# Optimization experiments

Measured on AMD Instinct MI355X. Metric: run time of the kernel, lower is better.

The kernel has to match this reference:

```python
import jax, jax.numpy as jnp
import numpy as np

N, E, F, H, A, C, NC, L, AH = 50000, 800000, 768, 256, 128, 128, 7, 2, 4

def _ln(x, g, b):
    m = jnp.mean(x, axis=-1, keepdims=True)
    v = jnp.var(x, axis=-1, keepdims=True)
    return (x - m) / jnp.sqrt(v + 1e-5) * g + b

def setup_inputs() -> dict:
    key = jax.random.key(0)
    ks = jax.random.split(key, 32)
    s = 0.02
    d = {}
    d['x'] = jax.random.normal(ks[0], (N, F), jnp.float32)
    d['edge_index'] = jax.random.randint(ks[1], (2, E), 0, N, jnp.int32)
    d['W_in'] = jax.random.normal(ks[2], (F, H), jnp.float32) * s
    d['b_in'] = jnp.zeros((H,), jnp.float32)
    d['gin_W1'] = jax.random.normal(ks[3], (L, H, H), jnp.float32) * s
    d['gin_b1'] = jnp.zeros((L, H), jnp.float32)
    d['gin_lng'] = jnp.ones((L, H), jnp.float32)
    d['gin_lnb'] = jnp.zeros((L, H), jnp.float32)
    d['gin_W2'] = jax.random.normal(ks[4], (L, H, H), jnp.float32) * s
    d['gin_b2'] = jnp.zeros((L, H), jnp.float32)
    d['eps'] = jnp.zeros((L,), jnp.float32)
    d['ln_g'] = jnp.ones((L, H), jnp.float32)
    d['ln_b'] = jnp.zeros((L, H), jnp.float32)
    d['att_W1'] = jax.random.normal(ks[5], (AH, H, A), jnp.float32) * s
    d['att_b1'] = jnp.zeros((AH, A), jnp.float32)
    d['att_W2'] = jax.random.normal(ks[6], (AH, A), jnp.float32) * s
    d['att_b2'] = jnp.zeros((AH,), jnp.float32)
    d['Wc1'] = jax.random.normal(ks[7], (H, C), jnp.float32) * s
    d['bc1'] = jnp.zeros((C,), jnp.float32)
    d['lnc1_g'] = jnp.ones((C,), jnp.float32)
    d['lnc1_b'] = jnp.zeros((C,), jnp.float32)
    d['Wc2'] = jax.random.normal(ks[8], (C, C // 2), jnp.float32) * s
    d['bc2'] = jnp.zeros((C // 2,), jnp.float32)
    d['lnc2_g'] = jnp.ones((C // 2,), jnp.float32)
    d['lnc2_b'] = jnp.zeros((C // 2,), jnp.float32)
    d['Wc3'] = jax.random.normal(ks[9], (C // 2, NC), jnp.float32) * s
    d['bc3'] = jnp.zeros((NC,), jnp.float32)
    return d

def reference(x, edge_index, W_in, b_in, gin_W1, gin_b1, gin_lng, gin_lnb, gin_W2, gin_b2, eps, ln_g, ln_b, att_W1, att_b1, att_W2, att_b2, Wc1, bc1, lnc1_g, lnc1_b, Wc2, bc2, lnc2_g, lnc2_b, Wc3, bc3):
    src, dst = edge_index[0], edge_index[1]
    # input projection (use_residual and input_dim != gnn_hidden)
    h = x @ W_in + b_in  # [N,H]
    for i in range(L):
        agg = jax.ops.segment_sum(h[src], dst, num_segments=N)  # GIN sum aggregation
        m = (1.0 + eps[i]) * h + agg
        m = _ln(m @ gin_W1[i] + gin_b1[i], gin_lng[i], gin_lnb[i])
        m = jax.nn.relu(m) @ gin_W2[i] + gin_b2[i]
        hn = jax.nn.relu(_ln(m, ln_g[i], ln_b[i]))
        h = hn + h  # residual (shapes match)
    # multi-head attention pooling, softmax over node dim
    s = jnp.tanh(jnp.einsum('nd,kda->kna', h, att_W1) + att_b1[:, None, :])  # [AH,N,A]
    logits = jnp.einsum('kna,ka->kn', s, att_W2) + att_b2[:, None]  # [AH,N]
    a = jax.nn.softmax(logits, axis=1)  # [AH,N]
    z = jnp.einsum('kn,nd->kd', a, h)  # [AH,H]
    z_agg = jnp.mean(z, axis=0)  # [H]
    attn = a.T  # [N,AH]
    # classifier (full variant)
    c = jax.nn.relu(_ln(z_agg @ Wc1 + bc1, lnc1_g, lnc1_b))
    c = jax.nn.relu(_ln(c @ Wc2 + bc2, lnc2_g, lnc2_b))
    probs = jax.nn.softmax(c @ Wc3 + bc3, axis=0)
    return probs, attn
```

## Files before the change

### kernel.cpp

```cpp
#include <hip/hip_runtime.h>
#include <math.h>

#define NN 50000
#define NE 800000
#define FF 768
#define HH 256

typedef __attribute__((ext_vector_type(8))) short short8;
typedef __attribute__((ext_vector_type(4))) float f32x4;

__device__ inline unsigned short f2bf(float f) {
  unsigned u = __float_as_uint(f);
  u = u + 0x7fffu + ((u >> 16) & 1u);
  return (unsigned short)(u >> 16);
}
__device__ inline float bf2f(unsigned short b) {
  return __uint_as_float(((unsigned)b) << 16);
}

__global__ void k_count(const int* __restrict__ dstv, int* __restrict__ deg) {
  int e = blockIdx.x * 256 + threadIdx.x;
  if (e < NE) atomicAdd(&deg[dstv[e]], 1);
}

__global__ void k_scan(const int* __restrict__ deg, int* __restrict__ rowptr) {
  const int CH = 49;
  int tid = threadIdx.x;
  int lane = tid & 63, w = tid >> 6;
  int base = tid * CH;
  int sum = 0;
  for (int i = 0; i < CH; i++) {
    int idx = base + i;
    if (idx < NN) sum += deg[idx];
  }
  int incl = sum;
  for (int off = 1; off < 64; off <<= 1) {
    int tv = __shfl_up(incl, off, 64);
    if (lane >= off) incl += tv;
  }
  __shared__ int ws[16];
  if (lane == 63) ws[w] = incl;
  __syncthreads();
  if (tid == 0) {
    int c = 0;
    for (int i = 0; i < 16; i++) { int tv = ws[i]; ws[i] = c; c += tv; }
  }
  __syncthreads();
  int run = ws[w] + (incl - sum);
  if (tid == 0) rowptr[0] = 0;
  for (int i = 0; i < CH; i++) {
    int idx = base + i;
    if (idx < NN) { run += deg[idx]; rowptr[idx + 1] = run; }
  }
}

__global__ void k_scatter(const int* __restrict__ srcv, const int* __restrict__ dstv,
                          int* __restrict__ cursor, int* __restrict__ csr_src) {
  int e = blockIdx.x * 256 + threadIdx.x;
  if (e < NE) {
    int d = dstv[e];
    int pos = atomicAdd(&cursor[d], 1);
    csr_src[pos] = srcv[e];
  }
}

__global__ void k_agg(const unsigned short* __restrict__ hb, const int* __restrict__ rowptr,
                      const int* __restrict__ csr_src, const float* __restrict__ eps,
                      int layer, unsigned short* __restrict__ mb) {
  int node = (blockIdx.x * blockDim.x + threadIdx.x) >> 6;
  int lane = threadIdx.x & 63;
  if (node >= NN) return;
  int beg = rowptr[node], end = rowptr[node + 1];
  const ushort4* hv = (const ushort4*)hb;
  float ax = 0.f, ay = 0.f, az = 0.f, aw = 0.f;
  for (int e = beg; e < end; ++e) {
    int s = csr_src[e];
    ushort4 v = hv[(size_t)s * 64 + lane];
    ax += bf2f(v.x); ay += bf2f(v.y); az += bf2f(v.z); aw += bf2f(v.w);
  }
  float ep = 1.0f + eps[layer];
  ushort4 h0 = hv[(size_t)node * 64 + lane];
  ax += ep * bf2f(h0.x); ay += ep * bf2f(h0.y);
  az += ep * bf2f(h0.z); aw += ep * bf2f(h0.w);
  ushort4 o;
  o.x = f2bf(ax); o.y = f2bf(ay); o.z = f2bf(az); o.w = f2bf(aw);
  *(ushort4*)&mb[(size_t)node * 256 + lane * 4] = o;
}

__global__ void k_tcast(const float* __restrict__ src0, unsigned short* __restrict__ dst0,
                        int R, int C) {
  const float* src = src0 + (size_t)blockIdx.z * R * C;
  unsigned short* dst = dst0 + (size_t)blockIdx.z * R * C;
  __shared__ float tile[32][33];
  int bx = blockIdx.x * 32, by = blockIdx.y * 32;
  int tx = threadIdx.x & 31, ty = threadIdx.x >> 5;
  for (int i = 0; i < 32; i += 8) {
    int r = by + ty + i, c = bx + tx;
    tile[ty + i][tx] = (r < R && c < C) ? src[(size_t)r * C + c] : 0.f;
  }
  __syncthreads();
  for (int i = 0; i < 32; i += 8) {
    int c = bx + ty + i, r = by + tx;
    if (c < C && r < R) dst[(size_t)c * R + r] = f2bf(tile[tx][ty + i]);
  }
}

__global__ __launch_bounds__(256) void k_mmff(
    const float* __restrict__ x, const unsigned short* __restrict__ Bt,
    const float* __restrict__ bias, float* __restrict__ outf,
    unsigned short* __restrict__ outb) {
  __shared__ unsigned short As[64 * 264];
  int t = threadIdx.x, lane = t & 63, wave = t >> 6;
  int row0 = blockIdx.x * 64;
  int m16 = lane & 15, kq = lane >> 4;
  f32x4 acc[4][4];
#pragma unroll
  for (int i = 0; i < 4; i++)
#pragma unroll
    for (int j = 0; j < 4; j++) acc[i][j] = (f32x4)(0.f);
  int sr = t >> 5;
  int sc = (t & 31) * 8;

  for (int kc = 0; kc < FF; kc += 256) {
    if (kc) __syncthreads();
#pragma unroll
    for (int j = 0; j < 8; j++) {
      int rr = j * 8 + sr;
      int gr = row0 + rr; if (gr >= NN) gr = NN - 1;
      const float* xp = x + (size_t)gr * FF + kc + sc;
      float4 f0 = *(const float4*)xp;
      float4 f1 = *(const float4*)(xp + 4);
      short8 v;
      v[0] = (short)f2bf(f0.x); v[1] = (short)f2bf(f0.y);
      v[2] = (short)f2bf(f0.z); v[3] = (short)f2bf(f0.w);
      v[4] = (short)f2bf(f1.x); v[5] = (short)f2bf(f1.y);
      v[6] = (short)f2bf(f1.z); v[7] = (short)f2bf(f1.w);
      *(short8*)&As[rr * 264 + sc] = v;
    }
    __syncthreads();
#pragma unroll
    for (int k0 = 0; k0 < 256; k0 += 32) {
      short8 a[4], b[4];
#pragma unroll
      for (int rt = 0; rt < 4; rt++)
        a[rt] = *(const short8*)&As[(rt * 16 + m16) * 264 + k0 + kq * 8];
#pragma unroll
      for (int ct = 0; ct < 4; ct++)
        b[ct] = *(const short8*)&Bt[(size_t)(wave * 64 + ct * 16 + m16) * FF + kc + k0 + kq * 8];
#pragma unroll
      for (int rt = 0; rt < 4; rt++)
#pragma unroll
        for (int ct = 0; ct < 4; ct++)
          acc[rt][ct] = __builtin_amdgcn_mfma_f32_16x16x32_bf16(a[rt], b[ct], acc[rt][ct], 0, 0, 0);
    }
  }
  int colbase = wave * 64 + m16;
  float bv[4];
#pragma unroll
  for (int ct = 0; ct < 4; ct++) bv[ct] = bias[colbase + ct * 16];
#pragma unroll
  for (int rt = 0; rt < 4; rt++)
#pragma unroll
    for (int reg = 0; reg < 4; reg++) {
      int r = row0 + rt * 16 + kq * 4 + reg;
      if (r < NN) {
#pragma unroll
        for (int ct = 0; ct < 4; ct++) {
          float v = acc[rt][ct][reg] + bv[ct];
          outf[(size_t)r * 256 + colbase + ct * 16] = v;
          outb[(size_t)r * 256 + colbase + ct * 16] = f2bf(v);
        }
      }
    }
}

template <int EPI, bool WF>
__global__ __launch_bounds__(256) void k_mmh(
    const unsigned short* __restrict__ Ab, const unsigned short* __restrict__ Bt,
    const float* __restrict__ bias, const float* __restrict__ g,
    const float* __restrict__ be, const float* __restrict__ resid,
    float* __restrict__ outf, unsigned short* __restrict__ outb) {
  __shared__ unsigned short As[64 * 264];
  __shared__ float redS[4][64];
  __shared__ float redQ[4][64];
  __shared__ float mvM[64], mvI[64];
  int t = threadIdx.x, lane = t & 63, wave = t >> 6;
  int row0 = blockIdx.x * 64;
  int sr = t >> 5, sc = (t & 31) * 8;
#pragma unroll
  for (int j = 0; j < 8; j++) {
    int rr = j * 8 + sr;
    int gr = row0 + rr; if (gr >= NN) gr = NN - 1;
    *(float4*)&As[rr * 264 + sc] = *(const float4*)&Ab[(size_t)gr * 256 + sc];
  }
  __syncthreads();
  int m16 = lane & 15, kq = lane >> 4;
  f32x4 acc[4][4];
#pragma unroll
  for (int i = 0; i < 4; i++)
#pragma unroll
    for (int j = 0; j < 4; j++) acc[i][j] = (f32x4)(0.f);
#pragma unroll
  for (int k0 = 0; k0 < 256; k0 += 32) {
    short8 a[4], b[4];
#pragma unroll
    for (int rt = 0; rt < 4; rt++)
      a[rt] = *(const short8*)&As[(rt * 16 + m16) * 264 + k0 + kq * 8];
#pragma unroll
    for (int ct = 0; ct < 4; ct++)
      b[ct] = *(const short8*)&Bt[(size_t)(wave * 64 + ct * 16 + m16) * 256 + k0 + kq * 8];
#pragma unroll
    for (int rt = 0; rt < 4; rt++)
#pragma unroll
      for (int ct = 0; ct < 4; ct++)
        acc[rt][ct] = __builtin_amdgcn_mfma_f32_16x16x32_bf16(a[rt], b[ct], acc[rt][ct], 0, 0, 0);
  }

  int colbase = wave * 64 + m16;
  float bv[4];
#pragma unroll
  for (int ct = 0; ct < 4; ct++) bv[ct] = bias[colbase + ct * 16];

  float s[4][4], q[4][4];
#pragma unroll
  for (int rt = 0; rt < 4; rt++)
#pragma unroll
    for (int reg = 0; reg < 4; reg++) { s[rt][reg] = 0.f; q[rt][reg] = 0.f; }
#pragma unroll
  for (int rt = 0; rt < 4; rt++)
#pragma unroll
    for (int ct = 0; ct < 4; ct++)
#pragma unroll
      for (int reg = 0; reg < 4; reg++) {
        float v = acc[rt][ct][reg] + bv[ct];
        acc[rt][ct][reg] = v;
        s[rt][reg] += v;
        q[rt][reg] += v * v;
      }
#pragma unroll
  for (int off = 1; off < 16; off <<= 1) {
#pragma unroll
    for (int rt = 0; rt < 4; rt++)
#pragma unroll
      for (int reg = 0; reg < 4; reg++) {
        s[rt][reg] += __shfl_xor(s[rt][reg], off, 64);
        q[rt][reg] += __shfl_xor(q[rt][reg], off, 64);
      }
  }
  if (m16 == 0) {
#pragma unroll
    for (int rt = 0; rt < 4; rt++)
#pragma unroll
      for (int reg = 0; reg < 4; reg++) {
        redS[wave][rt * 16 + kq * 4 + reg] = s[rt][reg];
        redQ[wave][rt * 16 + kq * 4 + reg] = q[rt][reg];
      }
  }
  __syncthreads();
  if (t < 64) {
    float ss = redS[0][t] + redS[1][t] + redS[2][t] + redS[3][t];
    float qq = redQ[0][t] + redQ[1][t] + redQ[2][t] + redQ[3][t];
    float mean = ss * (1.f / 256.f);
    float var = qq * (1.f / 256.f) - mean * mean;
    mvM[t] = mean;
    mvI[t] = rsqrtf(var + 1e-5f);
  }
  __syncthreads();
  float gv[4], bev[4];
#pragma unroll
  for (int ct = 0; ct < 4; ct++) { gv[ct] = g[colbase + ct * 16]; bev[ct] = be[colbase + ct * 16]; }
#pragma unroll
  for (int rt = 0; rt < 4; rt++)
#pragma unroll
    for (int reg = 0; reg < 4; reg++) {
      int rr = rt * 16 + kq * 4 + reg;
      int r = row0 + rr;
      if (r >= NN) continue;
      float mean = mvM[rr], inv = mvI[rr];
#pragma unroll
      for (int ct = 0; ct < 4; ct++) {
        int col = colbase + ct * 16;
        float val = fmaxf((acc[rt][ct][reg] - mean) * inv * gv[ct] + bev[ct], 0.f);
        if (EPI == 2) {
          val += resid[(size_t)r * 256 + col];
          if (WF) outf[(size_t)r * 256 + col] = val;
        }
        outb[(size_t)r * 256 + col] = f2bf(val);
      }
    }
}

__global__ __launch_bounds__(256) void k_att(const unsigned short* __restrict__ hb,
    const unsigned short* __restrict__ W1T, const float* __restrict__ b1,
    const float* __restrict__ W2, const float* __restrict__ b2,
    float* __restrict__ logitsT) {
  __shared__ unsigned short As[64 * 264];
  int t = threadIdx.x, lane = t & 63, wave = t >> 6;
  int row0 = blockIdx.x * 64;
  int sr = t >> 5, sc = (t & 31) * 8;
#pragma unroll
  for (int j = 0; j < 8; j++) {
    int rr = j * 8 + sr;
    int gr = row0 + rr; if (gr >= NN) gr = NN - 1;
    *(float4*)&As[rr * 264 + sc] = *(const float4*)&hb[(size_t)gr * 256 + sc];
  }
  __syncthreads();
  int m16 = lane & 15, kq = lane >> 4;
  f32x4 acc[4][8];
#pragma unroll
  for (int i = 0; i < 4; i++)
#pragma unroll
    for (int j = 0; j < 8; j++) acc[i][j] = (f32x4)(0.f);
#pragma unroll
  for (int k0 = 0; k0 < 256; k0 += 32) {
    short8 a[4];
#pragma unroll
    for (int rt = 0; rt < 4; rt++)
      a[rt] = *(const short8*)&As[(rt * 16 + m16) * 264 + k0 + kq * 8];
#pragma unroll
    for (int ct = 0; ct < 8; ct++) {
      short8 b = *(const short8*)&W1T[(size_t)(wave * 128 + ct * 16 + m16) * 256 + k0 + kq * 8];
#pragma unroll
      for (int rt = 0; rt < 4; rt++)
        acc[rt][ct] = __builtin_amdgcn_mfma_f32_16x16x32_bf16(a[rt], b, acc[rt][ct], 0, 0, 0);
    }
  }
  const float* b1k = b1 + wave * 128;
  const float* w2k = W2 + wave * 128;
  float p[4][4];
#pragma unroll
  for (int rt = 0; rt < 4; rt++)
#pragma unroll
    for (int reg = 0; reg < 4; reg++) p[rt][reg] = 0.f;
#pragma unroll
  for (int ct = 0; ct < 8; ct++) {
    int col = ct * 16 + m16;
    float b1v = b1k[col], w2v = w2k[col];
#pragma unroll
    for (int rt = 0; rt < 4; rt++)
#pragma unroll
      for (int reg = 0; reg < 4; reg++) {
        float xv = acc[rt][ct][reg] + b1v;
        xv = fminf(fmaxf(xv, -10.f), 10.f);
        float ex = __expf(2.f * xv);
        p[rt][reg] += (ex - 1.f) / (ex + 1.f) * w2v;
      }
  }
#pragma unroll
  for (int off = 1; off < 16; off <<= 1)
#pragma unroll
    for (int rt = 0; rt < 4; rt++)
#pragma unroll
      for (int reg = 0; reg < 4; reg++) p[rt][reg] += __shfl_xor(p[rt][reg], off, 64);
  if (m16 == 0) {
    float b2v = b2[wave];
#pragma unroll
    for (int rt = 0; rt < 4; rt++)
#pragma unroll
      for (int reg = 0; reg < 4; reg++) {
        int r = row0 + rt * 16 + kq * 4 + reg;
        if (r < NN) logitsT[(size_t)wave * NN + r] = p[rt][reg] + b2v;
      }
  }
}

__global__ void k_smax1(const float* __restrict__ logitsT, float* __restrict__ pmax,
                        float* __restrict__ psum) {
  int k = blockIdx.y;
  int tid = threadIdx.x;
  const float* L = logitsT + (size_t)k * NN;
  __shared__ float sm[256];
  float mx = -1e30f;
  for (int i = blockIdx.x * 256 + tid; i < NN; i += 128 * 256) mx = fmaxf(mx, L[i]);
  sm[tid] = mx; __syncthreads();
  for (int o = 128; o >= 1; o >>= 1) { if (tid < o) sm[tid] = fmaxf(sm[tid], sm[tid + o]); __syncthreads(); }
  float bmax = sm[0];
  __syncthreads();
  float s = 0.f;
  for (int i = blockIdx.x * 256 + tid; i < NN; i += 128 * 256) s += __expf(L[i] - bmax);
  sm[tid] = s; __syncthreads();
  for (int o = 128; o >= 1; o >>= 1) { if (tid < o) sm[tid] += sm[tid + o]; __syncthreads(); }
  if (tid == 0) { pmax[k * 128 + blockIdx.x] = bmax; psum[k * 128 + blockIdx.x] = sm[0]; }
}

__global__ void k_smax2(const float* __restrict__ pmax, const float* __restrict__ psum,
                        float* __restrict__ gs) {
  int k = blockIdx.x;
  int tid = threadIdx.x;
  __shared__ float sm[128], sv[128];
  float m = pmax[k * 128 + tid];
  sm[tid] = m; __syncthreads();
  for (int o = 64; o >= 1; o >>= 1) { if (tid < o) sm[tid] = fmaxf(sm[tid], sm[tid + o]); __syncthreads(); }
  float gm = sm[0];
  __syncthreads();
  sv[tid] = psum[k * 128 + tid] * __expf(m - gm);
  __syncthreads();
  for (int o = 64; o >= 1; o >>= 1) { if (tid < o) sv[tid] += sv[tid + o]; __syncthreads(); }
  if (tid == 0) { gs[k * 2] = gm; gs[k * 2 + 1] = sv[0]; }
}

__global__ void k_attnz(const float* __restrict__ logitsT, const float* __restrict__ gs,
                        const unsigned short* __restrict__ hb, float* __restrict__ out_attn,
                        float* __restrict__ z) {
  int n0 = blockIdx.x * 128;
  int tid = threadIdx.x;
  __shared__ float a[4][128];
  for (int i = tid; i < 512; i += 256) {
    int k = i >> 7, n = i & 127;
    float v = 0.f;
    if (n0 + n < NN) v = __expf(logitsT[(size_t)k * NN + n0 + n] - gs[k * 2]) / gs[k * 2 + 1];
    a[k][n] = v;
  }
  __syncthreads();
  for (int i = tid; i < 512; i += 256) {
    int n = i >> 2, k = i & 3;
    if (n0 + n < NN) out_attn[(size_t)(n0 + n) * 4 + k] = a[k][n];
  }
  float z0 = 0.f, z1 = 0.f, z2 = 0.f, z3 = 0.f;
  int d = tid;
  int nmax = NN - n0; if (nmax > 128) nmax = 128;
  for (int n = 0; n < nmax; n++) {
    float hv = bf2f(hb[(size_t)(n0 + n) * 256 + d]);
    z0 += a[0][n] * hv; z1 += a[1][n] * hv; z2 += a[2][n] * hv; z3 += a[3][n] * hv;
  }
  atomicAdd(&z[0 * 256 + d], z0);
  atomicAdd(&z[1 * 256 + d], z1);
  atomicAdd(&z[2 * 256 + d], z2);
  atomicAdd(&z[3 * 256 + d], z3);
}

__global__ void k_cls(const float* __restrict__ z, const float* __restrict__ Wc1,
                      const float* __restrict__ bc1, const float* __restrict__ g1,
                      const float* __restrict__ b1, const float* __restrict__ Wc2,
                      const float* __restrict__ bc2, const float* __restrict__ g2,
                      const float* __restrict__ b2, const float* __restrict__ Wc3,
                      const float* __restrict__ bc3, float* __restrict__ out) {
  int tid = threadIdx.x;
  __shared__ float za[256];
  __shared__ float buf[256];
  __shared__ float c1s[128];
  __shared__ float c2s[64];
  za[tid] = 0.25f * (z[tid] + z[256 + tid] + z[512 + tid] + z[768 + tid]);
  __syncthreads();
  float v1 = 0.f;
  if (tid < 128) {
    for (int d = 0; d < 256; d++) v1 += za[d] * Wc1[d * 128 + tid];
    v1 += bc1[tid];
  }
  buf[tid] = (tid < 128) ? v1 : 0.f; __syncthreads();
  for (int o = 128; o >= 1; o >>= 1) { if (tid < o) buf[tid] += buf[tid + o]; __syncthreads(); }
  float mean1 = buf[0] * (1.f / 128.f);
  __syncthreads();
  buf[tid] = (tid < 128) ? (v1 - mean1) * (v1 - mean1) : 0.f; __syncthreads();
  for (int o = 128; o >= 1; o >>= 1) { if (tid < o) buf[tid] += buf[tid + o]; __syncthreads(); }
  float inv1 = rsqrtf(buf[0] * (1.f / 128.f) + 1e-5f);
  __syncthreads();
  if (tid < 128) c1s[tid] = fmaxf((v1 - mean1) * inv1 * g1[tid] + b1[tid], 0.f);
  __syncthreads();
  float v2 = 0.f;
  if (tid < 64) {
    for (int d = 0; d < 128; d++) v2 += c1s[d] * Wc2[d * 64 + tid];
    v2 += bc2[tid];
  }
  buf[tid] = (tid < 64) ? v2 : 0.f; __syncthreads();
  for (int o = 128; o >= 1; o >>= 1) { if (tid < o) buf[tid] += buf[tid + o]; __syncthreads(); }
  float mean2 = buf[0] * (1.f / 64.f);
  __syncthreads();
  buf[tid] = (tid < 64) ? (v2 - mean2) * (v2 - mean2) : 0.f; __syncthreads();
  for (int o = 128; o >= 1; o >>= 1) { if (tid < o) buf[tid] += buf[tid + o]; __syncthreads(); }
  float inv2 = rsqrtf(buf[0] * (1.f / 64.f) + 1e-5f);
  __syncthreads();
  if (tid < 64) c2s[tid] = fmaxf((v2 - mean2) * inv2 * g2[tid] + b2[tid], 0.f);
  __syncthreads();
  if (tid < 7) {
    float l = 0.f;
    for (int d = 0; d < 64; d++) l += c2s[d] * Wc3[d * 7 + tid];
    buf[tid] = l + bc3[tid];
  }
  __syncthreads();
  if (tid == 0) {
    float mx = -1e30f;
    for (int i = 0; i < 7; i++) mx = fmaxf(mx, buf[i]);
    float s = 0.f;
    for (int i = 0; i < 7; i++) s += __expf(buf[i] - mx);
    for (int i = 0; i < 7; i++) out[i] = __expf(buf[i] - mx) / s;
  }
}

extern "C" void kernel_launch(void* const* d_in, const int* in_sizes, int n_in,
                              void* d_out, int out_size, void* d_ws, size_t ws_size,
                              hipStream_t stream) {
  const float* x       = (const float*)d_in[0];
  const int*   ei      = (const int*)d_in[1];
  const float* W_in    = (const float*)d_in[2];
  const float* b_in    = (const float*)d_in[3];
  const float* gin_W1  = (const float*)d_in[4];
  const float* gin_b1  = (const float*)d_in[5];
  const float* gin_lng = (const float*)d_in[6];
  const float* gin_lnb = (const float*)d_in[7];
  const float* gin_W2  = (const float*)d_in[8];
  const float* gin_b2  = (const float*)d_in[9];
  const float* eps     = (const float*)d_in[10];
  const float* ln_g    = (const float*)d_in[11];
  const float* ln_b    = (const float*)d_in[12];
  const float* att_W1  = (const float*)d_in[13];
  const float* att_b1  = (const float*)d_in[14];
  const float* att_W2  = (const float*)d_in[15];
  const float* att_b2  = (const float*)d_in[16];
  const float* Wc1     = (const float*)d_in[17];
  const float* bc1     = (const float*)d_in[18];
  const float* lnc1_g  = (const float*)d_in[19];
  const float* lnc1_b  = (const float*)d_in[20];
  const float* Wc2     = (const float*)d_in[21];
  const float* bc2     = (const float*)d_in[22];
  const float* lnc2_g  = (const float*)d_in[23];
  const float* lnc2_b  = (const float*)d_in[24];
  const float* Wc3     = (const float*)d_in[25];
  const float* bc3     = (const float*)d_in[26];
  float* out = (float*)d_out;
  (void)in_sizes; (void)n_in; (void)out_size; (void)ws_size;

  char* wsb = (char*)d_ws;
  size_t off = 0;
  auto alloc = [&](size_t bytes) {
    char* p = wsb + off;
    off += (bytes + 255) & ~(size_t)255;
    return p;
  };
  float*          h       = (float*)alloc((size_t)NN * HH * 4);
  unsigned short* hb      = (unsigned short*)alloc((size_t)NN * HH * 2);
  unsigned short* mb1     = (unsigned short*)alloc((size_t)NN * HH * 2);
  unsigned short* mb2     = (unsigned short*)alloc((size_t)NN * HH * 2);
  unsigned short* WinT    = (unsigned short*)alloc((size_t)HH * FF * 2);
  unsigned short* g1T     = (unsigned short*)alloc((size_t)2 * HH * HH * 2);
  unsigned short* g2T     = (unsigned short*)alloc((size_t)2 * HH * HH * 2);
  unsigned short* aW1T    = (unsigned short*)alloc((size_t)4 * 128 * HH * 2);
  float*          logitsT = (float*)alloc((size_t)4 * NN * 4);
  int*            deg     = (int*)alloc((size_t)NN * 4);
  int*            rowptr  = (int*)alloc((size_t)(NN + 1) * 4);
  int*            cursor  = (int*)alloc((size_t)NN * 4);
  int*            csr_src = (int*)alloc((size_t)NE * 4);
  float*          pmax    = (float*)alloc(4 * 128 * 4);
  float*          psum    = (float*)alloc(4 * 128 * 4);
  float*          gs      = (float*)alloc(8 * 4);
  float*          z       = (float*)alloc(4 * 256 * 4);

  const int* srcv = ei;
  const int* dstv = ei + NE;

  k_tcast<<<dim3((HH + 31) / 32, (FF + 31) / 32, 1), 256, 0, stream>>>(W_in, WinT, FF, HH);
  k_tcast<<<dim3(8, 8, 2), 256, 0, stream>>>(gin_W1, g1T, HH, HH);
  k_tcast<<<dim3(8, 8, 2), 256, 0, stream>>>(gin_W2, g2T, HH, HH);
  k_tcast<<<dim3(4, 8, 4), 256, 0, stream>>>(att_W1, aW1T, HH, 128);

  hipMemsetAsync(deg, 0, (size_t)NN * 4, stream);
  hipMemsetAsync(z, 0, 4 * 256 * 4, stream);
  k_count<<<(NE + 255) / 256, 256, 0, stream>>>(dstv, deg);
  k_scan<<<1, 1024, 0, stream>>>(deg, rowptr);
  hipMemcpyAsync(cursor, rowptr, (size_t)NN * 4, hipMemcpyDeviceToDevice, stream);
  k_scatter<<<(NE + 255) / 256, 256, 0, stream>>>(srcv, dstv, cursor, csr_src);

  int gblocks = (NN + 63) / 64;
  k_mmff<<<gblocks, 256, 0, stream>>>(x, WinT, b_in, h, hb);

  for (int l = 0; l < 2; l++) {
    k_agg<<<(NN + 3) / 4, 256, 0, stream>>>(hb, rowptr, csr_src, eps, l, mb1);
    k_mmh<1, true><<<gblocks, 256, 0, stream>>>(mb1, g1T + (size_t)l * HH * HH,
        gin_b1 + l * HH, gin_lng + l * HH, gin_lnb + l * HH, nullptr, nullptr, mb2);
    if (l == 0)
      k_mmh<2, true><<<gblocks, 256, 0, stream>>>(mb2, g2T + (size_t)l * HH * HH,
          gin_b2 + l * HH, ln_g + l * HH, ln_b + l * HH, h, h, hb);
    else
      k_mmh<2, false><<<gblocks, 256, 0, stream>>>(mb2, g2T + (size_t)l * HH * HH,
          gin_b2 + l * HH, ln_g + l * HH, ln_b + l * HH, h, nullptr, hb);
  }

  k_att<<<gblocks, 256, 0, stream>>>(hb, aW1T, att_b1, att_W2, att_b2, logitsT);
  k_smax1<<<dim3(128, 4), 256, 0, stream>>>(logitsT, pmax, psum);
  k_smax2<<<4, 128, 0, stream>>>(pmax, psum, gs);
  k_attnz<<<(NN + 127) / 128, 256, 0, stream>>>(logitsT, gs, hb, out + 7, z);
  k_cls<<<1, 256, 0, stream>>>(z, Wc1, bc1, lnc1_g, lnc1_b, Wc2, bc2, lnc2_g, lnc2_b,
                               Wc3, bc3, out);
}
```

Measured before the change: 1.010 ms.

## Fuse GIN MLP GEMMs and attention scoring into one kernel, stage B in LDS

Each GIN layer's two GEMMs, with their LayerNorm and ReLU epilogues, now run in one kernel that keeps the intermediate activation in LDS instead of writing and rereading mb2. The last layer also computes the attention logits from the same tile, so the separate k_att kernel and its reread of hb go away. Weight tiles are now staged through LDS, with an XOR swizzle in the fused kernel, and the next tile is register-prefetched while the current one is consumed. The input-projection GEMM is restructured the same way with 32-wide K chunks. This cuts global traffic and kernel launches, at the cost of more barriers per block and LDS atomics for the per-head logit reduction.

```diff
diff --git a/kernel.cpp b/kernel.cpp
--- a/kernel.cpp
+++ b/kernel.cpp
@@ -105,11 +105,12 @@
   }
 }
 
-__global__ __launch_bounds__(256) void k_mmff(
+__global__ __launch_bounds__(256) void k_mmff0(
     const float* __restrict__ x, const unsigned short* __restrict__ Bt,
     const float* __restrict__ bias, float* __restrict__ outf,
     unsigned short* __restrict__ outb) {
-  __shared__ unsigned short As[64 * 264];
+  __shared__ unsigned short As[64 * 40];
+  __shared__ unsigned short Bs[256 * 40];
   int t = threadIdx.x, lane = t & 63, wave = t >> 6;
   int row0 = blockIdx.x * 64;
   int m16 = lane & 15, kq = lane >> 4;
@@ -118,249 +119,361 @@
   for (int i = 0; i < 4; i++)
 #pragma unroll
     for (int j = 0; j < 4; j++) acc[i][j] = (f32x4)(0.f);
-  int sr = t >> 5;
-  int sc = (t & 31) * 8;
-
-  for (int kc = 0; kc < FF; kc += 256) {
-    if (kc) __syncthreads();
+  int arow = t >> 2, ac = t & 3;
+  int agr = row0 + arow; if (agr >= NN) agr = NN - 1;
+  float4 pa0, pa1, pb[4];
+  {
+    const float* Af = x + (size_t)agr * FF + ac * 8;
+    pa0 = *(const float4*)Af;
+    pa1 = *(const float4*)(Af + 4);
+#pragma unroll
+    for (int it = 0; it < 4; it++) {
+      int idx = t + it * 256;
+      int br = idx >> 2, bc = idx & 3;
+      pb[it] = *(const float4*)&Bt[(size_t)br * FF + bc * 8];
+    }
+  }
+  for (int kc = 0; kc < 24; kc++) {
+    short8 v;
+    v[0] = (short)f2bf(pa0.x); v[1] = (short)f2bf(pa0.y);
+    v[2] = (short)f2bf(pa0.z); v[3] = (short)f2bf(pa0.w);
+    v[4] = (short)f2bf(pa1.x); v[5] = (short)f2bf(pa1.y);
+    v[6] = (short)f2bf(pa1.z); v[7] = (short)f2bf(pa1.w);
+    *(short8*)&As[arow * 40 + ac * 8] = v;
+#pragma unroll
+    for (int it = 0; it < 4; it++) {
+      int idx = t + it * 256;
+      int br = idx >> 2, bc = idx & 3;
+      *(float4*)&Bs[br * 40 + bc * 8] = pb[it];
+    }
+    if (kc < 23) {
+      int k0 = (kc + 1) * 32;
+      const float* Af = x + (size_t)agr * FF + k0 + ac * 8;
+      pa0 = *(const float4*)Af;
+      pa1 = *(const float4*)(Af + 4);
+#pragma unroll
+      for (int it = 0; it < 4; it++) {
+        int idx = t + it * 256;
+        int br = idx >> 2, bc = idx & 3;
+        pb[it] = *(const float4*)&Bt[(size_t)br * FF + k0 + bc * 8];
+      }
+    }
+    __syncthreads();
+    short8 a[4], b[4];
+#pragma unroll
+    for (int rt = 0; rt < 4; rt++) a[rt] = *(const short8*)&As[(rt * 16 + m16) * 40 + kq * 8];
+#pragma unroll
+    for (int ct = 0; ct < 4; ct++)
+      b[ct] = *(const short8*)&Bs[(wave * 64 + ct * 16 + m16) * 40 + kq * 8];
+#pragma unroll
+    for (int rt = 0; rt < 4; rt++)
+#pragma unroll
+      for (int ct = 0; ct < 4; ct++)
+        acc[rt][ct] = __builtin_amdgcn_mfma_f32_16x16x32_bf16(a[rt], b[ct], acc[rt][ct], 0, 0, 0);
+    __syncthreads();
+  }
+  int colbase = wave * 64 + m16;
+  float bv[4];
+#pragma unroll
+  for (int ct = 0; ct < 4; ct++) bv[ct] = bias[colbase + ct * 16];
+#pragma unroll
+  for (int rt = 0; rt < 4; rt++)
+#pragma unroll
+    for (int reg = 0; reg < 4; reg++) {
+      int r = row0 + rt * 16 + kq * 4 + reg;
+      if (r < NN) {
+#pragma unroll
+        for (int ct = 0; ct < 4; ct++) {
+          float vv = acc[rt][ct][reg] + bv[ct];
+          outf[(size_t)r * 256 + colbase + ct * 16] = vv;
+          outb[(size_t)r * 256 + colbase + ct * 16] = f2bf(vv);
+        }
+      }
+    }
+}
+
+__device__ __forceinline__ void gemm_k256(
+    const unsigned short* __restrict__ Bt, const unsigned short* __restrict__ T1,
+    unsigned short* __restrict__ Bs, f32x4 (&acc)[4][4],
+    int t, int wave, int m16, int kq) {
+  int r4 = t >> 2, slot = t & 3;
+  float4 pf[4];
+#pragma unroll
+  for (int i = 0; i < 4; i++) {
+    int row = i * 64 + r4;
+    pf[i] = *(const float4*)&Bt[(size_t)row * 256 + slot * 8];
+  }
+#pragma unroll
+  for (int kc = 0; kc < 8; kc++) {
+#pragma unroll
+    for (int i = 0; i < 4; i++) {
+      int row = i * 64 + r4;
+      int s2 = slot ^ ((row >> 1) & 3);
+      *(float4*)((char*)Bs + row * 64 + s2 * 16) = pf[i];
+    }
+    if (kc < 7) {
+#pragma unroll
+      for (int i = 0; i < 4; i++) {
+        int row = i * 64 + r4;
+        pf[i] = *(const float4*)&Bt[(size_t)row * 256 + (kc + 1) * 32 + slot * 8];
+      }
+    }
+    __syncthreads();
+    short8 a[4], b[4];
+#pragma unroll
+    for (int rt = 0; rt < 4; rt++)
+      a[rt] = *(const short8*)&T1[(rt * 16 + m16) * 264 + kc * 32 + kq * 8];
+#pragma unroll
+    for (int ct = 0; ct < 4; ct++) {
+      int brow = wave * 64 + ct * 16 + m16;
+      int s2 = kq ^ ((brow >> 1) & 3);
+      b[ct] = *(const short8*)((const char*)Bs + brow * 64 + s2 * 16);
+    }
+#pragma unroll
+    for (int rt = 0; rt < 4; rt++)
+#pragma unroll
+      for (int ct = 0; ct < 4; ct++)
+        acc[rt][ct] = __builtin_amdgcn_mfma_f32_16x16x32_bf16(a[rt], b[ct], acc[rt][ct], 0, 0, 0);
+    __syncthreads();
+  }
+}
+
+template <bool WF, bool ATT>
+__global__ __launch_bounds__(256) void k_fused(
+    const unsigned short* __restrict__ Ab,
+    const unsigned short* __restrict__ B1t, const float* __restrict__ bias1,
+    const float* __restrict__ g1v, const float* __restrict__ be1,
+    const unsigned short* __restrict__ B2t, const float* __restrict__ bias2,
+    const float* __restrict__ g2v, const float* __restrict__ be2,
+    const float* __restrict__ resid, float* __restrict__ outf,
+    unsigned short* __restrict__ outb,
+    const unsigned short* __restrict__ aW1T, const float* __restrict__ ab1,
+    const float* __restrict__ aW2v, const float* __restrict__ ab2,
+    float* __restrict__ logitsT) {
+  __shared__ unsigned short T1[64 * 264];
+  __shared__ unsigned short Bs[256 * 32];
+  __shared__ float redS[4][64];
+  __shared__ float redQ[4][64];
+  __shared__ float mvM[64], mvI[64];
+  __shared__ float lg[4][64];
+  int t = threadIdx.x, lane = t & 63, wave = t >> 6;
+  int row0 = blockIdx.x * 64;
+  int m16 = lane & 15, kq = lane >> 4;
+  int colbase = wave * 64 + m16;
+
+  {
+    int sr = t >> 5, sc = (t & 31) * 8;
 #pragma unroll
     for (int j = 0; j < 8; j++) {
       int rr = j * 8 + sr;
       int gr = row0 + rr; if (gr >= NN) gr = NN - 1;
-      const float* xp = x + (size_t)gr * FF + kc + sc;
-      float4 f0 = *(const float4*)xp;
-      float4 f1 = *(const float4*)(xp + 4);
-      short8 v;
-      v[0] = (short)f2bf(f0.x); v[1] = (short)f2bf(f0.y);
-      v[2] = (short)f2bf(f0.z); v[3] = (short)f2bf(f0.w);
-      v[4] = (short)f2bf(f1.x); v[5] = (short)f2bf(f1.y);
-      v[6] = (short)f2bf(f1.z); v[7] = (short)f2bf(f1.w);
-      *(short8*)&As[rr * 264 + sc] = v;
-    }
-    __syncthreads();
-#pragma unroll
-    for (int k0 = 0; k0 < 256; k0 += 32) {
-      short8 a[4], b[4];
+      *(float4*)&T1[rr * 264 + sc] = *(const float4*)&Ab[(size_t)gr * 256 + sc];
+    }
+  }
+
+  f32x4 acc[4][4];
+#pragma unroll
+  for (int i = 0; i < 4; i++)
+#pragma unroll
+    for (int j = 0; j < 4; j++) acc[i][j] = (f32x4)(0.f);
+  gemm_k256(B1t, T1, Bs, acc, t, wave, m16, kq);
+
+  {
+    float bv[4];
+#pragma unroll
+    for (int ct = 0; ct < 4; ct++) bv[ct] = bias1[colbase + ct * 16];
+    float s[4][4], q[4][4];
+#pragma unroll
+    for (int rt = 0; rt < 4; rt++)
+#pragma unroll
+      for (int reg = 0; reg < 4; reg++) { s[rt][reg] = 0.f; q[rt][reg] = 0.f; }
+#pragma unroll
+    for (int rt = 0; rt < 4; rt++)
+#pragma unroll
+      for (int ct = 0; ct < 4; ct++)
+#pragma unroll
+        for (int reg = 0; reg < 4; reg++) {
+          float v = acc[rt][ct][reg] + bv[ct];
+          acc[rt][ct][reg] = v;
+          s[rt][reg] += v;
+          q[rt][reg] += v * v;
+        }
+#pragma unroll
+    for (int off = 1; off < 16; off <<= 1) {
 #pragma unroll
       for (int rt = 0; rt < 4; rt++)
-        a[rt] = *(const short8*)&As[(rt * 16 + m16) * 264 + k0 + kq * 8];
+#pragma unroll
+        for (int reg = 0; reg < 4; reg++) {
+          s[rt][reg] += __shfl_xor(s[rt][reg], off, 64);
+          q[rt][reg] += __shfl_xor(q[rt][reg], off, 64);
+        }
+    }
+    if (m16 == 0) {
+#pragma unroll
+      for (int rt = 0; rt < 4; rt++)
+#pragma unroll
+        for (int reg = 0; reg < 4; reg++) {
+          redS[wave][rt * 16 + kq * 4 + reg] = s[rt][reg];
+          redQ[wave][rt * 16 + kq * 4 + reg] = q[rt][reg];
+        }
+    }
+    __syncthreads();
+    if (t < 64) {
+      float ss = redS[0][t] + redS[1][t] + redS[2][t] + redS[3][t];
+      float qq = redQ[0][t] + redQ[1][t] + redQ[2][t] + redQ[3][t];
+      float mean = ss * (1.f / 256.f);
+      float var = qq * (1.f / 256.f) - mean * mean;
+      mvM[t] = mean;
+      mvI[t] = rsqrtf(var + 1e-5f);
+    }
+    __syncthreads();
+    float gv[4], bev[4];
+#pragma unroll
+    for (int ct = 0; ct < 4; ct++) { gv[ct] = g1v[colbase + ct * 16]; bev[ct] = be1[colbase + ct * 16]; }
+#pragma unroll
+    for (int rt = 0; rt < 4; rt++)
+#pragma unroll
+      for (int reg = 0; reg < 4; reg++) {
+        int rr = rt * 16 + kq * 4 + reg;
+        float mean = mvM[rr], inv = mvI[rr];
+#pragma unroll
+        for (int ct = 0; ct < 4; ct++) {
+          float val = fmaxf((acc[rt][ct][reg] - mean) * inv * gv[ct] + bev[ct], 0.f);
+          T1[rr * 264 + colbase + ct * 16] = f2bf(val);
+        }
+      }
+    __syncthreads();
+  }
+
+#pragma unroll
+  for (int i = 0; i < 4; i++)
+#pragma unroll
+    for (int j = 0; j < 4; j++) acc[i][j] = (f32x4)(0.f);
+  gemm_k256(B2t, T1, Bs, acc, t, wave, m16, kq);
+
+  {
+    float bv[4];
+#pragma unroll
+    for (int ct = 0; ct < 4; ct++) bv[ct] = bias2[colbase + ct * 16];
+    float s[4][4], q[4][4];
+#pragma unroll
+    for (int rt = 0; rt < 4; rt++)
+#pragma unroll
+      for (int reg = 0; reg < 4; reg++) { s[rt][reg] = 0.f; q[rt][reg] = 0.f; }
+#pragma unroll
+    for (int rt = 0; rt < 4; rt++)
 #pragma unroll
       for (int ct = 0; ct < 4; ct++)
-        b[ct] = *(const short8*)&Bt[(size_t)(wave * 64 + ct * 16 + m16) * FF + kc + k0 + kq * 8];
+#pragma unroll
+        for (int reg = 0; reg < 4; reg++) {
+          float v = acc[rt][ct][reg] + bv[ct];
+          acc[rt][ct][reg] = v;
+          s[rt][reg] += v;
+          q[rt][reg] += v * v;
+        }
+#pragma unroll
+    for (int off = 1; off < 16; off <<= 1) {
 #pragma unroll
       for (int rt = 0; rt < 4; rt++)
 #pragma unroll
-        for (int ct = 0; ct < 4; ct++)
-          acc[rt][ct] = __builtin_amdgcn_mfma_f32_16x16x32_bf16(a[rt], b[ct], acc[rt][ct], 0, 0, 0);
-    }
-  }
-  int colbase = wave * 64 + m16;
-  float bv[4];
-#pragma unroll
-  for (int ct = 0; ct < 4; ct++) bv[ct] = bias[colbase + ct * 16];
-#pragma unroll
-  for (int rt = 0; rt < 4; rt++)
-#pragma unroll
-    for (int reg = 0; reg < 4; reg++) {
-      int r = row0 + rt * 16 + kq * 4 + reg;
-      if (r < NN) {
+        for (int reg = 0; reg < 4; reg++) {
+          s[rt][reg] += __shfl_xor(s[rt][reg], off, 64);
+          q[rt][reg] += __shfl_xor(q[rt][reg], off, 64);
+        }
+    }
+    if (m16 == 0) {
+#pragma unroll
+      for (int rt = 0; rt < 4; rt++)
+#pragma unroll
+        for (int reg = 0; reg < 4; reg++) {
+          redS[wave][rt * 16 + kq * 4 + reg] = s[rt][reg];
+          redQ[wave][rt * 16 + kq * 4 + reg] = q[rt][reg];
+        }
+    }
+    __syncthreads();
+    if (t < 64) {
+      float ss = redS[0][t] + redS[1][t] + redS[2][t] + redS[3][t];
+      float qq = redQ[0][t] + redQ[1][t] + redQ[2][t] + redQ[3][t];
+      float mean = ss * (1.f / 256.f);
+      float var = qq * (1.f / 256.f) - mean * mean;
+      mvM[t] = mean;
+      mvI[t] = rsqrtf(var + 1e-5f);
+    }
+    __syncthreads();
+    float gv[4], bev[4];
+#pragma unroll
+    for (int ct = 0; ct < 4; ct++) { gv[ct] = g2v[colbase + ct * 16]; bev[ct] = be2[colbase + ct * 16]; }
+#pragma unroll
+    for (int rt = 0; rt < 4; rt++)
+#pragma unroll
+      for (int reg = 0; reg < 4; reg++) {
+        int rr = rt * 16 + kq * 4 + reg;
+        int r = row0 + rr;
+        float mean = mvM[rr], inv = mvI[rr];
 #pragma unroll
         for (int ct = 0; ct < 4; ct++) {
-          float v = acc[rt][ct][reg] + bv[ct];
-          outf[(size_t)r * 256 + colbase + ct * 16] = v;
-          outb[(size_t)r * 256 + colbase + ct * 16] = f2bf(v);
+          int col = colbase + ct * 16;
+          float val = fmaxf((acc[rt][ct][reg] - mean) * inv * gv[ct] + bev[ct], 0.f);
+          float rv = (r < NN) ? resid[(size_t)r * 256 + col] : 0.f;
+          val += rv;
+          if (r < NN) {
+            if (WF) outf[(size_t)r * 256 + col] = val;
+            outb[(size_t)r * 256 + col] = f2bf(val);
+          }
+          if (ATT) T1[rr * 264 + col] = f2bf(val);
         }
       }
-    }
-}
-
-template <int EPI, bool WF>
-__global__ __launch_bounds__(256) void k_mmh(
-    const unsigned short* __restrict__ Ab, const unsigned short* __restrict__ Bt,
-    const float* __restrict__ bias, const float* __restrict__ g,
-    const float* __restrict__ be, const float* __restrict__ resid,
-    float* __restrict__ outf, unsigned short* __restrict__ outb) {
-  __shared__ unsigned short As[64 * 264];
-  __shared__ float redS[4][64];
-  __shared__ float redQ[4][64];
-  __shared__ float mvM[64], mvI[64];
-  int t = threadIdx.x, lane = t & 63, wave = t >> 6;
-  int row0 = blockIdx.x * 64;
-  int sr = t >> 5, sc = (t & 31) * 8;
-#pragma unroll
-  for (int j = 0; j < 8; j++) {
-    int rr = j * 8 + sr;
-    int gr = row0 + rr; if (gr >= NN) gr = NN - 1;
-    *(float4*)&As[rr * 264 + sc] = *(const float4*)&Ab[(size_t)gr * 256 + sc];
-  }
-  __syncthreads();
-  int m16 = lane & 15, kq = lane >> 4;
-  f32x4 acc[4][4];
-#pragma unroll
-  for (int i = 0; i < 4; i++)
-#pragma unroll
-    for (int j = 0; j < 4; j++) acc[i][j] = (f32x4)(0.f);
-#pragma unroll
-  for (int k0 = 0; k0 < 256; k0 += 32) {
-    short8 a[4], b[4];
-#pragma unroll
-    for (int rt = 0; rt < 4; rt++)
-      a[rt] = *(const short8*)&As[(rt * 16 + m16) * 264 + k0 + kq * 8];
-#pragma unroll
-    for (int ct = 0; ct < 4; ct++)
-      b[ct] = *(const short8*)&Bt[(size_t)(wave * 64 + ct * 16 + m16) * 256 + k0 + kq * 8];
-#pragma unroll
-    for (int rt = 0; rt < 4; rt++)
-#pragma unroll
-      for (int ct = 0; ct < 4; ct++)
-        acc[rt][ct] = __builtin_amdgcn_mfma_f32_16x16x32_bf16(a[rt], b[ct], acc[rt][ct], 0, 0, 0);
-  }
-
-  int colbase = wave * 64 + m16;
-  float bv[4];
-#pragma unroll
-  for (int ct = 0; ct < 4; ct++) bv[ct] = bias[colbase + ct * 16];
-
-  float s[4][4], q[4][4];
-#pragma unroll
-  for (int rt = 0; rt < 4; rt++)
-#pragma unroll
-    for (int reg = 0; reg < 4; reg++) { s[rt][reg] = 0.f; q[rt][reg] = 0.f; }
-#pragma unroll
-  for (int rt = 0; rt < 4; rt++)
-#pragma unroll
-    for (int ct = 0; ct < 4; ct++)
-#pragma unroll
-      for (int reg = 0; reg < 4; reg++) {
-        float v = acc[rt][ct][reg] + bv[ct];
-        acc[rt][ct][reg] = v;
-        s[rt][reg] += v;
-        q[rt][reg] += v * v;
+  }
+
+  if (ATT) {
+    ((float*)lg)[t] = 0.f;
+#pragma unroll
+    for (int pass = 0; pass < 2; pass++) {
+#pragma unroll
+      for (int i = 0; i < 4; i++)
+#pragma unroll
+        for (int j = 0; j < 4; j++) acc[i][j] = (f32x4)(0.f);
+      gemm_k256(aW1T + (size_t)pass * 256 * 256, T1, Bs, acc, t, wave, m16, kq);
+      int head = pass * 2 + (wave >> 1);
+      const float* b1k = ab1 + head * 128;
+      const float* w2k = aW2v + head * 128;
+      float p[4][4];
+#pragma unroll
+      for (int rt = 0; rt < 4; rt++)
+#pragma unroll
+        for (int reg = 0; reg < 4; reg++) p[rt][reg] = 0.f;
+#pragma unroll
+      for (int ct = 0; ct < 4; ct++) {
+        int hcol = (wave & 1) * 64 + ct * 16 + m16;
+        float b1v = b1k[hcol], w2v = w2k[hcol];
+#pragma unroll
+        for (int rt = 0; rt < 4; rt++)
+#pragma unroll
+          for (int reg = 0; reg < 4; reg++) {
+            float xv = acc[rt][ct][reg] + b1v;
+            xv = fminf(fmaxf(xv, -10.f), 10.f);
+            float ex = __expf(2.f * xv);
+            p[rt][reg] += (ex - 1.f) / (ex + 1.f) * w2v;
+          }
       }
 #pragma unroll
-  for (int off = 1; off < 16; off <<= 1) {
-#pragma unroll
-    for (int rt = 0; rt < 4; rt++)
-#pragma unroll
-      for (int reg = 0; reg < 4; reg++) {
-        s[rt][reg] += __shfl_xor(s[rt][reg], off, 64);
-        q[rt][reg] += __shfl_xor(q[rt][reg], off, 64);
+      for (int off = 1; off < 16; off <<= 1)
+#pragma unroll
+        for (int rt = 0; rt < 4; rt++)
+#pragma unroll
+          for (int reg = 0; reg < 4; reg++) p[rt][reg] += __shfl_xor(p[rt][reg], off, 64);
+      if (m16 == 0) {
+#pragma unroll
+        for (int rt = 0; rt < 4; rt++)
+#pragma unroll
+          for (int reg = 0; reg < 4; reg++)
+            atomicAdd(&lg[head][rt * 16 + kq * 4 + reg], p[rt][reg]);
       }
-  }
-  if (m16 == 0) {
-#pragma unroll
-    for (int rt = 0; rt < 4; rt++)
-#pragma unroll
-      for (int reg = 0; reg < 4; reg++) {
-        redS[wave][rt * 16 + kq * 4 + reg] = s[rt][reg];
-        redQ[wave][rt * 16 + kq * 4 + reg] = q[rt][reg];
-      }
-  }
-  __syncthreads();
-  if (t < 64) {
-    float ss = redS[0][t] + redS[1][t] + redS[2][t] + redS[3][t];
-    float qq = redQ[0][t] + redQ[1][t] + redQ[2][t] + redQ[3][t];
-    float mean = ss * (1.f / 256.f);
-    float var = qq * (1.f / 256.f) - mean * mean;
-    mvM[t] = mean;
-    mvI[t] = rsqrtf(var + 1e-5f);
-  }
-  __syncthreads();
-  float gv[4], bev[4];
-#pragma unroll
-  for (int ct = 0; ct < 4; ct++) { gv[ct] = g[colbase + ct * 16]; bev[ct] = be[colbase + ct * 16]; }
-#pragma unroll
-  for (int rt = 0; rt < 4; rt++)
-#pragma unroll
-    for (int reg = 0; reg < 4; reg++) {
-      int rr = rt * 16 + kq * 4 + reg;
-      int r = row0 + rr;
-      if (r >= NN) continue;
-      float mean = mvM[rr], inv = mvI[rr];
-#pragma unroll
-      for (int ct = 0; ct < 4; ct++) {
-        int col = colbase + ct * 16;
-        float val = fmaxf((acc[rt][ct][reg] - mean) * inv * gv[ct] + bev[ct], 0.f);
-        if (EPI == 2) {
-          val += resid[(size_t)r * 256 + col];
-          if (WF) outf[(size_t)r * 256 + col] = val;
-        }
-        outb[(size_t)r * 256 + col] = f2bf(val);
-      }
-    }
-}
-
-__global__ __launch_bounds__(256) void k_att(const unsigned short* __restrict__ hb,
-    const unsigned short* __restrict__ W1T, const float* __restrict__ b1,
-    const float* __restrict__ W2, const float* __restrict__ b2,
-    float* __restrict__ logitsT) {
-  __shared__ unsigned short As[64 * 264];
-  int t = threadIdx.x, lane = t & 63, wave = t >> 6;
-  int row0 = blockIdx.x * 64;
-  int sr = t >> 5, sc = (t & 31) * 8;
-#pragma unroll
-  for (int j = 0; j < 8; j++) {
-    int rr = j * 8 + sr;
-    int gr = row0 + rr; if (gr >= NN) gr = NN - 1;
-    *(float4*)&As[rr * 264 + sc] = *(const float4*)&hb[(size_t)gr * 256 + sc];
-  }
-  __syncthreads();
-  int m16 = lane & 15, kq = lane >> 4;
-  f32x4 acc[4][8];
-#pragma unroll
-  for (int i = 0; i < 4; i++)
-#pragma unroll
-    for (int j = 0; j < 8; j++) acc[i][j] = (f32x4)(0.f);
-#pragma unroll
-  for (int k0 = 0; k0 < 256; k0 += 32) {
-    short8 a[4];
-#pragma unroll
-    for (int rt = 0; rt < 4; rt++)
-      a[rt] = *(const short8*)&As[(rt * 16 + m16) * 264 + k0 + kq * 8];
-#pragma unroll
-    for (int ct = 0; ct < 8; ct++) {
-      short8 b = *(const short8*)&W1T[(size_t)(wave * 128 + ct * 16 + m16) * 256 + k0 + kq * 8];
-#pragma unroll
-      for (int rt = 0; rt < 4; rt++)
-        acc[rt][ct] = __builtin_amdgcn_mfma_f32_16x16x32_bf16(a[rt], b, acc[rt][ct], 0, 0, 0);
-    }
-  }
-  const float* b1k = b1 + wave * 128;
-  const float* w2k = W2 + wave * 128;
-  float p[4][4];
-#pragma unroll
-  for (int rt = 0; rt < 4; rt++)
-#pragma unroll
-    for (int reg = 0; reg < 4; reg++) p[rt][reg] = 0.f;
-#pragma unroll
-  for (int ct = 0; ct < 8; ct++) {
-    int col = ct * 16 + m16;
-    float b1v = b1k[col], w2v = w2k[col];
-#pragma unroll
-    for (int rt = 0; rt < 4; rt++)
-#pragma unroll
-      for (int reg = 0; reg < 4; reg++) {
-        float xv = acc[rt][ct][reg] + b1v;
-        xv = fminf(fmaxf(xv, -10.f), 10.f);
-        float ex = __expf(2.f * xv);
-        p[rt][reg] += (ex - 1.f) / (ex + 1.f) * w2v;
-      }
-  }
-#pragma unroll
-  for (int off = 1; off < 16; off <<= 1)
-#pragma unroll
-    for (int rt = 0; rt < 4; rt++)
-#pragma unroll
-      for (int reg = 0; reg < 4; reg++) p[rt][reg] += __shfl_xor(p[rt][reg], off, 64);
-  if (m16 == 0) {
-    float b2v = b2[wave];
-#pragma unroll
-    for (int rt = 0; rt < 4; rt++)
-#pragma unroll
-      for (int reg = 0; reg < 4; reg++) {
-        int r = row0 + rt * 16 + kq * 4 + reg;
-        if (r < NN) logitsT[(size_t)wave * NN + r] = p[rt][reg] + b2v;
-      }
+    }
+    __syncthreads();
+    int hh = t >> 6, rr2 = t & 63;
+    int r = row0 + rr2;
+    if (r < NN) logitsT[(size_t)hh * NN + r] = lg[hh][rr2] + ab2[hh];
   }
 }
 
@@ -530,7 +643,6 @@
   float*          h       = (float*)alloc((size_t)NN * HH * 4);
   unsigned short* hb      = (unsigned short*)alloc((size_t)NN * HH * 2);
   unsigned short* mb1     = (unsigned short*)alloc((size_t)NN * HH * 2);
-  unsigned short* mb2     = (unsigned short*)alloc((size_t)NN * HH * 2);
   unsigned short* WinT    = (unsigned short*)alloc((size_t)HH * FF * 2);
   unsigned short* g1T     = (unsigned short*)alloc((size_t)2 * HH * HH * 2);
   unsigned short* g2T     = (unsigned short*)alloc((size_t)2 * HH * HH * 2);
@@ -561,21 +673,24 @@
   k_scatter<<<(NE + 255) / 256, 256, 0, stream>>>(srcv, dstv, cursor, csr_src);
 
   int gblocks = (NN + 63) / 64;
-  k_mmff<<<gblocks, 256, 0, stream>>>(x, WinT, b_in, h, hb);
+  k_mmff0<<<gblocks, 256, 0, stream>>>(x, WinT, b_in, h, hb);
 
   for (int l = 0; l < 2; l++) {
     k_agg<<<(NN + 3) / 4, 256, 0, stream>>>(hb, rowptr, csr_src, eps, l, mb1);
-    k_mmh<1, true><<<gblocks, 256, 0, stream>>>(mb1, g1T + (size_t)l * HH * HH,
-        gin_b1 + l * HH, gin_lng + l * HH, gin_lnb + l * HH, nullptr, nullptr, mb2);
+    const unsigned short* B1 = g1T + (size_t)l * HH * HH;
+    const unsigned short* B2 = g2T + (size_t)l * HH * HH;
     if (l == 0)
-      k_mmh<2, true><<<gblocks, 256, 0, stream>>>(mb2, g2T + (size_t)l * HH * HH,
-          gin_b2 + l * HH, ln_g + l * HH, ln_b + l * HH, h, h, hb);
+      k_fused<true, false><<<gblocks, 256, 0, stream>>>(
+          mb1, B1, gin_b1 + l * HH, gin_lng + l * HH, gin_lnb + l * HH,
+          B2, gin_b2 + l * HH, ln_g + l * HH, ln_b + l * HH,
+          h, h, hb, nullptr, nullptr, nullptr, nullptr, nullptr);
     else
-      k_mmh<2, false><<<gblocks, 256, 0, stream>>>(mb2, g2T + (size_t)l * HH * HH,
-          gin_b2 + l * HH, ln_g + l * HH, ln_b + l * HH, h, nullptr, hb);
-  }
-
-  k_att<<<gblocks, 256, 0, stream>>>(hb, aW1T, att_b1, att_W2, att_b2, logitsT);
+      k_fused<false, true><<<gblocks, 256, 0, stream>>>(
+          mb1, B1, gin_b1 + l * HH, gin_lng + l * HH, gin_lnb + l * HH,
+          B2, gin_b2 + l * HH, ln_g + l * HH, ln_b + l * HH,
+          h, h, hb, aW1T, att_b1, att_W2, att_b2, logitsT);
+  }
+
   k_smax1<<<dim3(128, 4), 256, 0, stream>>>(logitsT, pmax, psum);
   k_smax2<<<4, 128, 0, stream>>>(pmax, psum, gs);
   k_attnz<<<(NN + 127) / 128, 256, 0, stream>>>(logitsT, gs, hb, out + 7, z);
```

After: 1.172 ms. 16.0% more time.
